# Kernel tuning notes

Measured on AMD Instinct MI355X. Metric: run time of the kernel, lower is better.

The kernel has to match this reference:

```python
import jax, jax.numpy as jnp
import numpy as np

EPS = 1e-6
H = 8  # num_heads

def _ln(x, gamma, beta):
    mu = jnp.mean(x, axis=-1, keepdims=True)
    var = jnp.mean(jnp.square(x - mu), axis=-1, keepdims=True)
    return (x - mu) * jax.lax.rsqrt(var + EPS) * gamma + beta

def setup_inputs() -> dict:
    key = jax.random.key(0)
    ks = jax.random.split(key, 10)
    b, n_sink, n_src = 2, 1024, 4096
    sink_dim, src_dim, hid = 512, 512, 512
    s = 0.02
    return {
        "sink": jax.random.normal(ks[0], (b, n_sink, sink_dim), jnp.float32),
        "source": jax.random.normal(ks[1], (b, n_src, src_dim), jnp.float32),
        "gamma_s": jnp.ones((sink_dim,), jnp.float32),
        "beta_s": jnp.zeros((sink_dim,), jnp.float32),
        "gamma_c": jnp.ones((src_dim,), jnp.float32),
        "beta_c": jnp.zeros((src_dim,), jnp.float32),
        "Wq": jax.random.normal(ks[2], (sink_dim, hid), jnp.float32) * s,
        "bq": jnp.zeros((hid,), jnp.float32),
        "Wkv": jax.random.normal(ks[3], (src_dim, 2 * hid), jnp.float32) * s,
        "bkv": jnp.zeros((2 * hid,), jnp.float32),
        "Wo": jax.random.normal(ks[4], (hid, sink_dim), jnp.float32) * s,
        "bo": jnp.zeros((sink_dim,), jnp.float32),
    }

def reference(sink, source, gamma_s, beta_s, gamma_c, beta_c, Wq, bq, Wkv, bkv, Wo, bo):
    b, n_sink, _ = sink.shape
    n_src = source.shape[1]
    hid = Wq.shape[1]
    d = hid // H
    scale = d ** -0.5
    # pre-norm
    s = _ln(sink, gamma_s, beta_s)
    c = _ln(source, gamma_c, beta_c)
    # projections -> [b, h, n, d]
    q = (s @ Wq + bq).reshape(b, n_sink, H, d).transpose(0, 2, 1, 3)
    kv = c @ Wkv + bkv
    k, v = jnp.split(kv, 2, axis=-1)
    k = k.reshape(b, n_src, H, d).transpose(0, 2, 1, 3)
    v = v.reshape(b, n_src, H, d).transpose(0, 2, 1, 3)
    sim = jnp.einsum('bhid,bhjd->bhij', q, k) * scale  # [b,h,i,j]
    # sink competition: softmax over query axis i, then renormalize over keys j
    attn = jax.nn.softmax(sim, axis=-2) + EPS
    attn = attn / jnp.sum(attn, axis=-1, keepdims=True)
    out = jnp.einsum('bhij,bhjd->bhid', attn, v)
    out = out.transpose(0, 2, 1, 3).reshape(b, n_sink, hid)
    return out @ Wo + bo
```

## Files before the change

kernel.cpp:

```cpp
#include <hip/hip_runtime.h>
#include <hip/hip_bf16.h>
#include <math.h>

#define EPS 1e-6f
#define NSINK 1024
#define NSRC 4096
#define DIM 512
#define NH 8
#define HD 64
#define BATCH 2
#define VROWS 65
#define QSCALE 0.18033688011112042f

typedef unsigned short u16;
typedef __attribute__((ext_vector_type(8))) short short8;
typedef __attribute__((ext_vector_type(4))) float f32x4;

__device__ inline float fast_exp2(float x) {
#if __has_builtin(__builtin_amdgcn_exp2f)
    return __builtin_amdgcn_exp2f(x);
#else
    return exp2f(x);
#endif
}
__device__ inline float fast_rcp(float x) {
#if __has_builtin(__builtin_amdgcn_rcpf)
    return __builtin_amdgcn_rcpf(x);
#else
    return 1.0f / x;
#endif
}
__device__ inline u16 f2bf(float x) {
    union { float f; unsigned u; } v; v.f = x;
    unsigned r = v.u + 0x7fffu + ((v.u >> 16) & 1u);
    return (u16)(r >> 16);
}
__device__ inline float bf2f(u16 h) {
    union { unsigned u; float f; } v; v.u = ((unsigned)h) << 16;
    return v.f;
}
__device__ inline unsigned pk_bf16(float a, float b) {
    union { __hip_bfloat162 h; unsigned u; } v;
    v.h = __float22bfloat162_rn(make_float2(a, b));
    return v.u;
}
__device__ inline f32x4 mfma16(short8 a, short8 b, f32x4 c) {
    return __builtin_amdgcn_mfma_f32_16x16x32_bf16(a, b, c, 0, 0, 0);
}
__device__ inline short8 ldfrag(const u16* base, int stride, int lane) {
    return *(const short8*)(base + (size_t)(lane & 15) * stride + ((lane >> 4) << 3));
}

__device__ inline void gld16(const u16* g, u16* l) {
    __builtin_amdgcn_global_load_lds(
        (const __attribute__((address_space(1))) unsigned*)g,
        (__attribute__((address_space(3))) unsigned*)l, 16, 0, 0);
}

template<int TM>
__device__ inline void stage_tile(u16* lds, const u16* gsrc, int K, int t) {
    #pragma unroll
    for (int it = 0; it < TM / 32; ++it) {
        int m = it * 32 + (t >> 3);
        int c = (t & 7) ^ (m & 7);
        gld16(gsrc + (size_t)m * K + c * 8,
              lds + it * 2048 + (t >> 6) * 512);
    }
}
__device__ inline short8 rdfrag(const u16* tile, int fbase, int cbase, int lane) {
    int m = fbase + (lane & 15);
    int c = (cbase + (lane >> 4)) ^ (m & 7);
    return *(const short8*)(tile + (size_t)m * 64 + c * 8);
}

__global__ __launch_bounds__(256) void ln_all(
    const float* __restrict__ sink, const float* __restrict__ source,
    const float* __restrict__ gs, const float* __restrict__ bs,
    const float* __restrict__ gc, const float* __restrict__ bc,
    u16* __restrict__ sh, u16* __restrict__ ch)
{
    int row = blockIdx.x;
    const float* xr; const float* g; const float* be; u16* y;
    if (row < BATCH * NSINK) {
        xr = sink + (size_t)row * DIM; g = gs; be = bs; y = sh + (size_t)row * DIM;
    } else {
        int rr = row - BATCH * NSINK;
        xr = source + (size_t)rr * DIM; g = gc; be = bc; y = ch + (size_t)rr * DIM;
    }
    int t = threadIdx.x;
    float v0 = xr[t], v1 = xr[t + 256];
    float s = v0 + v1, sq = v0 * v0 + v1 * v1;
    #pragma unroll
    for (int off = 32; off > 0; off >>= 1) {
        s  += __shfl_down(s, off, 64);
        sq += __shfl_down(sq, off, 64);
    }
    __shared__ float rsm[4], rq[4];
    int wave = t >> 6;
    if ((t & 63) == 0) { rsm[wave] = s; rq[wave] = sq; }
    __syncthreads();
    s  = rsm[0] + rsm[1] + rsm[2] + rsm[3];
    sq = rq[0] + rq[1] + rq[2] + rq[3];
    float mu = s * (1.0f / DIM);
    float var = sq * (1.0f / DIM) - mu * mu;
    float a = var + EPS;
    float r = rsqrtf(a);
    r = r * (1.5f - 0.5f * a * r * r);
    y[t]       = f2bf((v0 - mu) * r * g[t] + be[t]);
    y[t + 256] = f2bf((v1 - mu) * r * g[t + 256] + be[t + 256]);
}

__global__ __launch_bounds__(256) void wt_all(
    const float* __restrict__ Wq, const float* __restrict__ Wkv, const float* __restrict__ Wo,
    u16* __restrict__ wqT, u16* __restrict__ wkvT, u16* __restrict__ woT)
{
    int n = blockIdx.x;
    const float* W; u16* T; int N; int nn;
    if (n < 512)       { W = Wq;  T = wqT;  N = 512;  nn = n; }
    else if (n < 1536) { W = Wkv; T = wkvT; N = 1024; nn = n - 512; }
    else               { W = Wo;  T = woT;  N = 512;  nn = n - 1536; }
    for (int k = threadIdx.x; k < 512; k += 256)
        T[(size_t)nn * 512 + k] = f2bf(W[(size_t)k * N + nn]);
}

template<int MODE, int TM, int TN, int SWZ>
__global__ __launch_bounds__(256) void gemm1(
    const u16* __restrict__ A, const u16* __restrict__ BT,
    const float* __restrict__ bias, int K,
    float* __restrict__ cf, u16* __restrict__ o1, u16* __restrict__ o2)
{
    constexpr int FM = TM / 32, FN = TN / 32;
    __shared__ u16 As[2][TM * 64];
    __shared__ u16 Bs[2][TN * 64];
    int t = threadIdx.x;
    int wave = t >> 6, lane = t & 63;
    int wr = wave >> 1, wc = wave & 1;
    int m0, n0;
    if constexpr (SWZ) {
        int id = blockIdx.x;
        int slot = id >> 3;
        m0 = ((id & 7) * 8 + (slot & 7)) * TM;
        n0 = (slot >> 3) * TN;
    } else {
        m0 = blockIdx.y * TM;
        n0 = blockIdx.x * TN;
    }

    f32x4 acc[FM][FN] = {};
    stage_tile<TM>(As[0], A + (size_t)m0 * K, K, t);
    stage_tile<TN>(Bs[0], BT + (size_t)n0 * K, K, t);
    __syncthreads();
    int nt = K >> 6;
    int cur = 0;
    for (int kt = 0; kt < nt; ++kt) {
        if (kt + 1 < nt) {
            stage_tile<TM>(As[cur ^ 1], A + (size_t)m0 * K + (kt + 1) * 64, K, t);
            stage_tile<TN>(Bs[cur ^ 1], BT + (size_t)n0 * K + (kt + 1) * 64, K, t);
        }
        #pragma unroll
        for (int kk = 0; kk < 2; ++kk) {
            short8 af[FM], bf[FN];
            #pragma unroll
            for (int f = 0; f < FM; ++f)
                af[f] = rdfrag(As[cur], wr * (TM / 2) + f * 16, kk * 4, lane);
            #pragma unroll
            for (int f = 0; f < FN; ++f)
                bf[f] = rdfrag(Bs[cur], wc * (TN / 2) + f * 16, kk * 4, lane);
            #pragma unroll
            for (int i = 0; i < FM; ++i)
                #pragma unroll
                for (int j = 0; j < FN; ++j)
                    acc[i][j] = mfma16(af[i], bf[j], acc[i][j]);
        }
        __syncthreads();
        cur ^= 1;
    }

    #pragma unroll
    for (int i = 0; i < FM; ++i)
        #pragma unroll
        for (int j = 0; j < FN; ++j)
            #pragma unroll
            for (int r = 0; r < 4; ++r) {
                int m = m0 + wr * (TM / 2) + i * 16 + (lane >> 4) * 4 + r;
                int n = n0 + wc * (TN / 2) + j * 16 + (lane & 15);
                float v = acc[i][j][r] + bias[n];
                if (MODE == 0) {
                    cf[(size_t)m * DIM + n] = v;
                } else if (MODE == 1) {
                    int b = m >> 10, ii = m & 1023;
                    int h = n >> 6, d = n & 63;
                    o1[((size_t)(b * NH + h) * NSINK + ii) * HD + d] = f2bf(v * QSCALE);
                } else {
                    int b = m >> 12, jj = m & 4095;
                    if (n < DIM) {
                        int h = n >> 6, d = n & 63;
                        o1[((size_t)(b * NH + h) * NSRC + jj) * HD + d] = f2bf(v);
                    } else {
                        int nn = n - DIM;
                        int h = nn >> 6, d = nn & 63;
                        o2[((size_t)(b * NH + h) * HD + d) * NSRC + jj] = f2bf(v);
                    }
                }
            }
}

__global__ __launch_bounds__(256, 4) void pass_a(const u16* __restrict__ q,
    const u16* __restrict__ k, float* __restrict__ part)
{
    int id = blockIdx.x;
    int slot = id >> 3;
    int bh = (id & 7) + 8 * (slot >> 6);
    int rem = slot & 63;
    int ic = rem >> 4;
    int t = threadIdx.x, wave = t >> 6, lane = t & 63;
    int j0 = (rem & 15) * 256 + wave * 64;
    const u16* qb = q + (size_t)bh * NSINK * HD;
    const u16* kb = k + (size_t)bh * NSRC * HD;

    __shared__ u16 Qs[2][64 * 64];

    short8 kf[4][2];
    #pragma unroll
    for (int jf = 0; jf < 4; ++jf)
        #pragma unroll
        for (int kc = 0; kc < 2; ++kc)
            kf[jf][kc] = ldfrag(kb + (size_t)(j0 + jf * 16) * HD + kc * 32, HD, lane);

    float csum[4] = {};
    stage_tile<64>(Qs[0], qb + (size_t)(ic * 256) * HD, HD, t);
    __syncthreads();
    int cur = 0;
    for (int ii = 0; ii < 4; ++ii) {
        if (ii + 1 < 4)
            stage_tile<64>(Qs[cur ^ 1], qb + (size_t)(ic * 256 + (ii + 1) * 64) * HD, HD, t);
        #pragma unroll
        for (int f = 0; f < 4; ++f) {
            short8 q0 = rdfrag(Qs[cur], f * 16, 0, lane);
            short8 q1 = rdfrag(Qs[cur], f * 16, 4, lane);
            f32x4 s[4] = {};
            #pragma unroll
            for (int jf = 0; jf < 4; ++jf) s[jf] = mfma16(q0, kf[jf][0], s[jf]);
            #pragma unroll
            for (int jf = 0; jf < 4; ++jf) s[jf] = mfma16(q1, kf[jf][1], s[jf]);
            #pragma unroll
            for (int jf = 0; jf < 4; ++jf)
                csum[jf] += fast_exp2(s[jf][0]) + fast_exp2(s[jf][1])
                          + fast_exp2(s[jf][2]) + fast_exp2(s[jf][3]);
        }
        __syncthreads();
        cur ^= 1;
    }
    #pragma unroll
    for (int jf = 0; jf < 4; ++jf) {
        csum[jf] += __shfl_xor(csum[jf], 16, 64);
        csum[jf] += __shfl_xor(csum[jf], 32, 64);
    }
    if (lane < 16)
        #pragma unroll
        for (int jf = 0; jf < 4; ++jf)
            part[((size_t)ic * BATCH * NH + bh) * NSRC + j0 + jf * 16 + lane] = csum[jf];
}

__global__ __launch_bounds__(256) void vscale2(const u16* __restrict__ vTh,
    const float* __restrict__ cs_part, float* __restrict__ vs, u16* __restrict__ vT2)
{
    int d = blockIdx.x;
    int bh = blockIdx.y;
    const int S = BATCH * NH * NSRC;
    const float* cp = cs_part + (size_t)bh * NSRC;
    u16* dst = vT2 + ((size_t)bh * VROWS + d) * NSRC;
    if (d == 64) {
        for (int j = threadIdx.x; j < NSRC; j += 256) {
            float cs = cp[j] + cp[j + S] + cp[j + 2 * S] + cp[j + 3 * S];
            dst[j] = f2bf(fast_rcp(cs));
        }
        return;
    }
    const u16* src = vTh + ((size_t)bh * HD + d) * NSRC;
    float acc = 0.f;
    for (int j = threadIdx.x; j < NSRC; j += 256) {
        float v = bf2f(src[j]);
        acc += v;
        float cs = cp[j] + cp[j + S] + cp[j + 2 * S] + cp[j + 3 * S];
        dst[j] = f2bf(v * fast_rcp(cs));
    }
    #pragma unroll
    for (int off = 32; off > 0; off >>= 1) acc += __shfl_down(acc, off, 64);
    __shared__ float r4[4];
    if ((threadIdx.x & 63) == 0) r4[threadIdx.x >> 6] = acc;
    __syncthreads();
    if (threadIdx.x == 0) vs[bh * HD + d] = r4[0] + r4[1] + r4[2] + r4[3];
}

__global__ __launch_bounds__(256, 3) void pass_b(const u16* __restrict__ q,
    const u16* __restrict__ k, const u16* __restrict__ vT2,
    float* __restrict__ pv, float* __restrict__ rs)
{
    int id = blockIdx.x;
    int slot = id >> 3;
    int bh = (id & 7) + 8 * (slot >> 5);
    int rem = slot & 31;
    int split = rem >> 3;
    int i0 = (rem & 7) * 128;
    int t = threadIdx.x, wave = t >> 6, lane = t & 63;
    const u16* qb = q + (size_t)bh * NSINK * HD;
    const u16* kb = k + (size_t)bh * NSRC * HD;
    const u16* vb = vT2 + (size_t)bh * VROWS * NSRC;

    __shared__ u16 Ks[2][64 * 64];
    __shared__ u16 Vs[2][64 * 64];
    __shared__ alignas(16) u16 Rcs[2][64];
    __shared__ alignas(16) u16 pbuf[4][2][16 * 76];

    short8 qf[2][2];
    #pragma unroll
    for (int fi = 0; fi < 2; ++fi)
        #pragma unroll
        for (int kc = 0; kc < 2; ++kc)
            qf[fi][kc] = ldfrag(qb + (size_t)(i0 + wave * 32 + fi * 16) * HD + kc * 32, HD, lane);

    auto stage = [&](int buf, int jt) {
        int j0 = split * (NSRC / 4) + jt * 64;
        stage_tile<64>(Ks[buf], kb + (size_t)j0 * HD, HD, t);
        stage_tile<64>(Vs[buf], vb + j0, NSRC, t);
        if (t < 8) gld16(vb + (size_t)64 * NSRC + j0 + t * 8, Rcs[buf]);
    };

    f32x4 o[2][5] = {};
    stage(0, 0);
    __syncthreads();
    int cur = 0;
    for (int jt = 0; jt < 16; ++jt) {
        if (jt + 1 < 16) stage(cur ^ 1, jt + 1);
        f32x4 s[2][4] = {};
        #pragma unroll
        for (int kc = 0; kc < 2; ++kc)
            #pragma unroll
            for (int jf = 0; jf < 4; ++jf) {
                short8 kf = rdfrag(Ks[cur], jf * 16, kc * 4, lane);
                s[0][jf] = mfma16(kf, qf[0][kc], s[0][jf]);
                s[1][jf] = mfma16(kf, qf[1][kc], s[1][jf]);
            }
        #pragma unroll
        for (int fi = 0; fi < 2; ++fi)
            #pragma unroll
            for (int jf = 0; jf < 4; ++jf) {
                uint2 w;
                w.x = pk_bf16(fast_exp2(s[fi][jf][0]), fast_exp2(s[fi][jf][1]));
                w.y = pk_bf16(fast_exp2(s[fi][jf][2]), fast_exp2(s[fi][jf][3]));
                *(uint2*)&pbuf[wave][fi][(size_t)(lane & 15) * 76 + jf * 16 + (lane >> 4) * 4] = w;
            }
        short8 z = {};
        #pragma unroll
        for (int jc = 0; jc < 2; ++jc) {
            short8 pa0 = *(const short8*)&pbuf[wave][0][(size_t)(lane & 15) * 76 + jc * 32 + (lane >> 4) * 8];
            short8 pa1 = *(const short8*)&pbuf[wave][1][(size_t)(lane & 15) * 76 + jc * 32 + (lane >> 4) * 8];
            #pragma unroll
            for (int df = 0; df < 4; ++df) {
                short8 vf = rdfrag(Vs[cur], df * 16, jc * 4, lane);
                o[0][df] = mfma16(pa0, vf, o[0][df]);
                o[1][df] = mfma16(pa1, vf, o[1][df]);
            }
            short8 b5 = z;
            if ((lane & 15) == 0)
                b5 = *(const short8*)&Rcs[cur][jc * 32 + (lane >> 4) * 8];
            o[0][4] = mfma16(pa0, b5, o[0][4]);
            o[1][4] = mfma16(pa1, b5, o[1][4]);
        }
        __syncthreads();
        cur ^= 1;
    }
    if ((lane & 15) == 0) {
        #pragma unroll
        for (int fi = 0; fi < 2; ++fi)
            #pragma unroll
            for (int r = 0; r < 4; ++r)
                rs[((size_t)split * (BATCH * NH) + bh) * NSINK + i0 + wave * 32 + fi * 16 + (lane >> 4) * 4 + r] = o[fi][4][r];
    }
    int b = bh >> 3, h = bh & 7;
    float* pvp = pv + (size_t)split * BATCH * NSINK * DIM;
    #pragma unroll
    for (int fi = 0; fi < 2; ++fi)
        #pragma unroll
        for (int df = 0; df < 4; ++df)
            #pragma unroll
            for (int r = 0; r < 4; ++r) {
                int row = i0 + wave * 32 + fi * 16 + (lane >> 4) * 4 + r;
                pvp[((size_t)(b * NSINK + row)) * DIM + h * HD + df * 16 + (lane & 15)] = o[fi][df][r];
            }
}

__global__ __launch_bounds__(256) void finalize_pv(const float* __restrict__ pv,
    const float* __restrict__ rs, const float* __restrict__ vs,
    u16* __restrict__ ab)
{
    const int M = BATCH * NSINK * DIM;
    const int R = BATCH * NH * NSINK;
    int idx = blockIdx.x * 256 + threadIdx.x;
    int m = idx >> 9, n = idx & 511;
    int b = m >> 10, i = m & 1023, h = n >> 6, d = n & 63;
    int bh = b * NH + h;
    float val = pv[idx] + pv[idx + M] + pv[idx + 2 * M] + pv[idx + 3 * M]
              + EPS * vs[bh * HD + d];
    float rsv = rs[bh * NSINK + i] + rs[R + bh * NSINK + i]
              + rs[2 * R + bh * NSINK + i] + rs[3 * R + bh * NSINK + i]
              + (float)NSRC * EPS;
    ab[idx] = f2bf(val / rsv);
}

extern "C" void kernel_launch(void* const* d_in, const int* in_sizes, int n_in,
                              void* d_out, int out_size, void* d_ws, size_t ws_size,
                              hipStream_t stream) {
    (void)in_sizes; (void)n_in; (void)out_size;
    const float* sink    = (const float*)d_in[0];
    const float* source  = (const float*)d_in[1];
    const float* gamma_s = (const float*)d_in[2];
    const float* beta_s  = (const float*)d_in[3];
    const float* gamma_c = (const float*)d_in[4];
    const float* beta_c  = (const float*)d_in[5];
    const float* Wq      = (const float*)d_in[6];
    const float* bq      = (const float*)d_in[7];
    const float* Wkv     = (const float*)d_in[8];
    const float* bkv     = (const float*)d_in[9];
    const float* Wo      = (const float*)d_in[10];
    const float* bo      = (const float*)d_in[11];
    float* out = (float*)d_out;

    char* p = (char*)d_ws;
    auto carve = [&](size_t bytes) { char* r = p; p += (bytes + 255) & ~(size_t)255; return r; };
    u16* sh    = (u16*)carve(2048ull * 512 * 2);
    u16* ch    = (u16*)carve(8192ull * 512 * 2);
    u16* wqT   = (u16*)carve(512ull * 512 * 2);
    u16* wkvT  = (u16*)carve(1024ull * 512 * 2);
    u16* woT   = (u16*)carve(512ull * 512 * 2);
    u16* qb    = (u16*)carve(16ull * 1024 * 64 * 2);
    u16* kb    = (u16*)carve(16ull * 4096 * 64 * 2);
    u16* vTh   = (u16*)carve(16ull * 64 * 4096 * 2);
    u16* vT2   = (u16*)carve(16ull * VROWS * 4096 * 2);
    float* cs_part = (float*)carve(4ull * 16 * 4096 * 4);
    float* vs      = (float*)carve(1024ull * 4);
    float* rs      = (float*)carve(4ull * 16 * 1024 * 4);
    float* pv      = (float*)carve(4ull * 2048 * 512 * 4);
    u16*   ab      = (u16*)carve(2048ull * 512 * 2);
    if ((size_t)(p - (char*)d_ws) > ws_size) return;

    ln_all<<<BATCH * (NSINK + NSRC), 256, 0, stream>>>(
        sink, source, gamma_s, beta_s, gamma_c, beta_c, sh, ch);
    wt_all<<<2048, 256, 0, stream>>>(Wq, Wkv, Wo, wqT, wkvT, woT);

    gemm1<1, 64, 64, 0><<<dim3(DIM / 64, BATCH * NSINK / 64), 256, 0, stream>>>(
        sh, wqT, bq, 512, nullptr, qb, nullptr);
    gemm1<2, 128, 128, 1><<<512, 256, 0, stream>>>(
        ch, wkvT, bkv, 512, nullptr, kb, vTh);

    pass_a<<<1024, 256, 0, stream>>>(qb, kb, cs_part);
    vscale2<<<dim3(VROWS, BATCH * NH), 256, 0, stream>>>(vTh, cs_part, vs, vT2);
    pass_b<<<512, 256, 0, stream>>>(qb, kb, vT2, pv, rs);
    finalize_pv<<<4096, 256, 0, stream>>>(pv, rs, vs, ab);

    gemm1<0, 64, 64, 0><<<dim3(DIM / 64, BATCH * NSINK / 64), 256, 0, stream>>>(
        ab, woT, bo, 512, out, nullptr, nullptr);
}
```

Before: 111.6 us.

## Fuse prep kernels, use permlane for P fragments, store partial PV in bf16

```diff
diff --git a/kernel.cpp b/kernel.cpp
--- a/kernel.cpp
+++ b/kernel.cpp
@@ -12,6 +12,12 @@
 #define VROWS 65
 #define QSCALE 0.18033688011112042f
 
+#if __has_builtin(__builtin_amdgcn_permlane32_swap) && __has_builtin(__builtin_amdgcn_permlane16_swap)
+#define HAVE_PERMLANE 1
+#else
+#define HAVE_PERMLANE 0
+#endif
+
 typedef unsigned short u16;
 typedef __attribute__((ext_vector_type(8))) short short8;
 typedef __attribute__((ext_vector_type(4))) float f32x4;
@@ -73,13 +79,43 @@
     return *(const short8*)(tile + (size_t)m * 64 + c * 8);
 }
 
-__global__ __launch_bounds__(256) void ln_all(
+#if HAVE_PERMLANE
+__device__ inline short8 pa_frag(const f32x4 sA, const f32x4 sB) {
+    unsigned A0 = pk_bf16(sA[0], sA[1]);
+    unsigned A1 = pk_bf16(sA[2], sA[3]);
+    unsigned B0 = pk_bf16(sB[0], sB[1]);
+    unsigned B1 = pk_bf16(sB[2], sB[3]);
+    auto c0 = __builtin_amdgcn_permlane32_swap(A0, B0, false, false);
+    auto c1 = __builtin_amdgcn_permlane32_swap(A1, B1, false, false);
+    auto d0 = __builtin_amdgcn_permlane16_swap(c0[0], c0[1], false, false);
+    auto d1 = __builtin_amdgcn_permlane16_swap(c1[0], c1[1], false, false);
+    union { unsigned u[4]; short8 s8; } r;
+    r.u[0] = d0[0]; r.u[1] = d1[0]; r.u[2] = d0[1]; r.u[3] = d1[1];
+    return r.s8;
+}
+#endif
+
+__global__ __launch_bounds__(256) void prep(
     const float* __restrict__ sink, const float* __restrict__ source,
     const float* __restrict__ gs, const float* __restrict__ bs,
     const float* __restrict__ gc, const float* __restrict__ bc,
-    u16* __restrict__ sh, u16* __restrict__ ch)
+    const float* __restrict__ Wq, const float* __restrict__ Wkv,
+    const float* __restrict__ Wo,
+    u16* __restrict__ sh, u16* __restrict__ ch,
+    u16* __restrict__ wqT, u16* __restrict__ wkvT, u16* __restrict__ woT)
 {
     int row = blockIdx.x;
+    int t = threadIdx.x;
+    if (row >= BATCH * (NSINK + NSRC)) {
+        int n = row - BATCH * (NSINK + NSRC);
+        const float* W; u16* T; int N; int nn;
+        if (n < 512)       { W = Wq;  T = wqT;  N = 512;  nn = n; }
+        else if (n < 1536) { W = Wkv; T = wkvT; N = 1024; nn = n - 512; }
+        else               { W = Wo;  T = woT;  N = 512;  nn = n - 1536; }
+        for (int k = t; k < 512; k += 256)
+            T[(size_t)nn * 512 + k] = f2bf(W[(size_t)k * N + nn]);
+        return;
+    }
     const float* xr; const float* g; const float* be; u16* y;
     if (row < BATCH * NSINK) {
         xr = sink + (size_t)row * DIM; g = gs; be = bs; y = sh + (size_t)row * DIM;
@@ -87,7 +123,6 @@
         int rr = row - BATCH * NSINK;
         xr = source + (size_t)rr * DIM; g = gc; be = bc; y = ch + (size_t)rr * DIM;
     }
-    int t = threadIdx.x;
     float v0 = xr[t], v1 = xr[t + 256];
     float s = v0 + v1, sq = v0 * v0 + v1 * v1;
     #pragma unroll
@@ -108,19 +143,6 @@
     r = r * (1.5f - 0.5f * a * r * r);
     y[t]       = f2bf((v0 - mu) * r * g[t] + be[t]);
     y[t + 256] = f2bf((v1 - mu) * r * g[t + 256] + be[t + 256]);
-}
-
-__global__ __launch_bounds__(256) void wt_all(
-    const float* __restrict__ Wq, const float* __restrict__ Wkv, const float* __restrict__ Wo,
-    u16* __restrict__ wqT, u16* __restrict__ wkvT, u16* __restrict__ woT)
-{
-    int n = blockIdx.x;
-    const float* W; u16* T; int N; int nn;
-    if (n < 512)       { W = Wq;  T = wqT;  N = 512;  nn = n; }
-    else if (n < 1536) { W = Wkv; T = wkvT; N = 1024; nn = n - 512; }
-    else               { W = Wo;  T = woT;  N = 512;  nn = n - 1536; }
-    for (int k = threadIdx.x; k < 512; k += 256)
-        T[(size_t)nn * 512 + k] = f2bf(W[(size_t)k * N + nn]);
 }
 
 template<int MODE, int TM, int TN, int SWZ>
@@ -262,19 +284,24 @@
             part[((size_t)ic * BATCH * NH + bh) * NSRC + j0 + jf * 16 + lane] = csum[jf];
 }
 
+__global__ __launch_bounds__(256) void csred(const float* __restrict__ part,
+    float* __restrict__ rcs)
+{
+    int x = blockIdx.x * 256 + threadIdx.x;
+    const int S = BATCH * NH * NSRC;
+    float cs = part[x] + part[x + S] + part[x + 2 * S] + part[x + 3 * S];
+    rcs[x] = fast_rcp(cs);
+}
+
 __global__ __launch_bounds__(256) void vscale2(const u16* __restrict__ vTh,
-    const float* __restrict__ cs_part, float* __restrict__ vs, u16* __restrict__ vT2)
+    const float* __restrict__ rcs, float* __restrict__ vs, u16* __restrict__ vT2)
 {
     int d = blockIdx.x;
     int bh = blockIdx.y;
-    const int S = BATCH * NH * NSRC;
-    const float* cp = cs_part + (size_t)bh * NSRC;
+    const float* rc = rcs + (size_t)bh * NSRC;
     u16* dst = vT2 + ((size_t)bh * VROWS + d) * NSRC;
     if (d == 64) {
-        for (int j = threadIdx.x; j < NSRC; j += 256) {
-            float cs = cp[j] + cp[j + S] + cp[j + 2 * S] + cp[j + 3 * S];
-            dst[j] = f2bf(fast_rcp(cs));
-        }
+        for (int j = threadIdx.x; j < NSRC; j += 256) dst[j] = f2bf(rc[j]);
         return;
     }
     const u16* src = vTh + ((size_t)bh * HD + d) * NSRC;
@@ -282,8 +309,7 @@
     for (int j = threadIdx.x; j < NSRC; j += 256) {
         float v = bf2f(src[j]);
         acc += v;
-        float cs = cp[j] + cp[j + S] + cp[j + 2 * S] + cp[j + 3 * S];
-        dst[j] = f2bf(v * fast_rcp(cs));
+        dst[j] = f2bf(v * rc[j]);
     }
     #pragma unroll
     for (int off = 32; off > 0; off >>= 1) acc += __shfl_down(acc, off, 64);
@@ -295,7 +321,7 @@
 
 __global__ __launch_bounds__(256, 3) void pass_b(const u16* __restrict__ q,
     const u16* __restrict__ k, const u16* __restrict__ vT2,
-    float* __restrict__ pv, float* __restrict__ rs)
+    u16* __restrict__ pvb, float* __restrict__ rs)
 {
     int id = blockIdx.x;
     int slot = id >> 3;
@@ -311,7 +337,9 @@
     __shared__ u16 Ks[2][64 * 64];
     __shared__ u16 Vs[2][64 * 64];
     __shared__ alignas(16) u16 Rcs[2][64];
+#if !HAVE_PERMLANE
     __shared__ alignas(16) u16 pbuf[4][2][16 * 76];
+#endif
 
     short8 qf[2][2];
     #pragma unroll
@@ -345,17 +373,31 @@
         #pragma unroll
         for (int fi = 0; fi < 2; ++fi)
             #pragma unroll
+            for (int jf = 0; jf < 4; ++jf)
+                #pragma unroll
+                for (int r = 0; r < 4; ++r)
+                    s[fi][jf][r] = fast_exp2(s[fi][jf][r]);
+#if !HAVE_PERMLANE
+        #pragma unroll
+        for (int fi = 0; fi < 2; ++fi)
+            #pragma unroll
             for (int jf = 0; jf < 4; ++jf) {
                 uint2 w;
-                w.x = pk_bf16(fast_exp2(s[fi][jf][0]), fast_exp2(s[fi][jf][1]));
-                w.y = pk_bf16(fast_exp2(s[fi][jf][2]), fast_exp2(s[fi][jf][3]));
+                w.x = pk_bf16(s[fi][jf][0], s[fi][jf][1]);
+                w.y = pk_bf16(s[fi][jf][2], s[fi][jf][3]);
                 *(uint2*)&pbuf[wave][fi][(size_t)(lane & 15) * 76 + jf * 16 + (lane >> 4) * 4] = w;
             }
+#endif
         short8 z = {};
         #pragma unroll
         for (int jc = 0; jc < 2; ++jc) {
+#if HAVE_PERMLANE
+            short8 pa0 = pa_frag(s[0][2 * jc], s[0][2 * jc + 1]);
+            short8 pa1 = pa_frag(s[1][2 * jc], s[1][2 * jc + 1]);
+#else
             short8 pa0 = *(const short8*)&pbuf[wave][0][(size_t)(lane & 15) * 76 + jc * 32 + (lane >> 4) * 8];
             short8 pa1 = *(const short8*)&pbuf[wave][1][(size_t)(lane & 15) * 76 + jc * 32 + (lane >> 4) * 8];
+#endif
             #pragma unroll
             for (int df = 0; df < 4; ++df) {
                 short8 vf = rdfrag(Vs[cur], df * 16, jc * 4, lane);
@@ -379,7 +421,7 @@
                 rs[((size_t)split * (BATCH * NH) + bh) * NSINK + i0 + wave * 32 + fi * 16 + (lane >> 4) * 4 + r] = o[fi][4][r];
     }
     int b = bh >> 3, h = bh & 7;
-    float* pvp = pv + (size_t)split * BATCH * NSINK * DIM;
+    u16* pvp = pvb + (size_t)split * BATCH * NSINK * DIM;
     #pragma unroll
     for (int fi = 0; fi < 2; ++fi)
         #pragma unroll
@@ -387,11 +429,11 @@
             #pragma unroll
             for (int r = 0; r < 4; ++r) {
                 int row = i0 + wave * 32 + fi * 16 + (lane >> 4) * 4 + r;
-                pvp[((size_t)(b * NSINK + row)) * DIM + h * HD + df * 16 + (lane & 15)] = o[fi][df][r];
+                pvp[((size_t)(b * NSINK + row)) * DIM + h * HD + df * 16 + (lane & 15)] = f2bf(o[fi][df][r]);
             }
 }
 
-__global__ __launch_bounds__(256) void finalize_pv(const float* __restrict__ pv,
+__global__ __launch_bounds__(256) void finalize_pv(const u16* __restrict__ pvb,
     const float* __restrict__ rs, const float* __restrict__ vs,
     u16* __restrict__ ab)
 {
@@ -401,8 +443,8 @@
     int m = idx >> 9, n = idx & 511;
     int b = m >> 10, i = m & 1023, h = n >> 6, d = n & 63;
     int bh = b * NH + h;
-    float val = pv[idx] + pv[idx + M] + pv[idx + 2 * M] + pv[idx + 3 * M]
-              + EPS * vs[bh * HD + d];
+    float val = bf2f(pvb[idx]) + bf2f(pvb[idx + M]) + bf2f(pvb[idx + 2 * M])
+              + bf2f(pvb[idx + 3 * M]) + EPS * vs[bh * HD + d];
     float rsv = rs[bh * NSINK + i] + rs[R + bh * NSINK + i]
               + rs[2 * R + bh * NSINK + i] + rs[3 * R + bh * NSINK + i]
               + (float)NSRC * EPS;
@@ -439,15 +481,16 @@
     u16* vTh   = (u16*)carve(16ull * 64 * 4096 * 2);
     u16* vT2   = (u16*)carve(16ull * VROWS * 4096 * 2);
     float* cs_part = (float*)carve(4ull * 16 * 4096 * 4);
+    float* rcs     = (float*)carve(16ull * 4096 * 4);
     float* vs      = (float*)carve(1024ull * 4);
     float* rs      = (float*)carve(4ull * 16 * 1024 * 4);
-    float* pv      = (float*)carve(4ull * 2048 * 512 * 4);
+    u16*   pvb     = (u16*)carve(4ull * 2048 * 512 * 2);
     u16*   ab      = (u16*)carve(2048ull * 512 * 2);
     if ((size_t)(p - (char*)d_ws) > ws_size) return;
 
-    ln_all<<<BATCH * (NSINK + NSRC), 256, 0, stream>>>(
-        sink, source, gamma_s, beta_s, gamma_c, beta_c, sh, ch);
-    wt_all<<<2048, 256, 0, stream>>>(Wq, Wkv, Wo, wqT, wkvT, woT);
+    prep<<<BATCH * (NSINK + NSRC) + 2048, 256, 0, stream>>>(
+        sink, source, gamma_s, beta_s, gamma_c, beta_c,
+        Wq, Wkv, Wo, sh, ch, wqT, wkvT, woT);
 
     gemm1<1, 64, 64, 0><<<dim3(DIM / 64, BATCH * NSINK / 64), 256, 0, stream>>>(
         sh, wqT, bq, 512, nullptr, qb, nullptr);
@@ -455,9 +498,10 @@
         ch, wkvT, bkv, 512, nullptr, kb, vTh);
 
     pass_a<<<1024, 256, 0, stream>>>(qb, kb, cs_part);
-    vscale2<<<dim3(VROWS, BATCH * NH), 256, 0, stream>>>(vTh, cs_part, vs, vT2);
-    pass_b<<<512, 256, 0, stream>>>(qb, kb, vT2, pv, rs);
-    finalize_pv<<<4096, 256, 0, stream>>>(pv, rs, vs, ab);
+    csred<<<BATCH * NH * NSRC / 256, 256, 0, stream>>>(cs_part, rcs);
+    vscale2<<<dim3(VROWS, BATCH * NH), 256, 0, stream>>>(vTh, rcs, vs, vT2);
+    pass_b<<<512, 256, 0, stream>>>(qb, kb, vT2, pvb, rs);
+    finalize_pv<<<4096, 256, 0, stream>>>(pvb, rs, vs, ab);
 
     gemm1<0, 64, 64, 0><<<dim3(DIM / 64, BATCH * NSINK / 64), 256, 0, stream>>>(
         ab, woT, bo, 512, out, nullptr, nullptr);
```

Result: faster. 106.4 us (-4.7%).
